# Kernel optimization log

Measured on AMD Instinct MI355X. Metric: run time of the kernel, lower is better.

Reference implementation:

```python
import jax, jax.numpy as jnp
import numpy as np

STRIDES = [4, 8, 16, 32, 64]
SIZES = [32.0, 64.0, 128.0, 256.0, 512.0]
RATIOS = [0.5, 1.0, 2.0]
IMG = 1024.0
PRE_NMS = 1000
POST_NMS = 1000
NMS_THR = 0.7
MIN_SIZE = 0.0
SCALE_CLAMP = float(np.log(1000.0 / 16.0))
NEG = -1e4  # finite sentinel instead of -inf (keeps grads clean)


def conv(x, w, b, pad):
    y = jax.lax.conv_general_dilated(x, w, (1, 1), pad,
                                     dimension_numbers=('NCHW', 'OIHW', 'NCHW'))
    return y + b[None, :, None, None]


def gen_anchors(H, W, stride, size):
    # detectron2 cell anchors: w = size/sqrt(r), h = w*r, centered at shift
    rs = jnp.asarray(RATIOS, jnp.float32)
    ws = size / jnp.sqrt(rs)
    hs = ws * rs
    base = jnp.stack([-ws / 2, -hs / 2, ws / 2, hs / 2], -1)  # [A,4]
    sx = jnp.arange(W, dtype=jnp.float32) * stride
    sy = jnp.arange(H, dtype=jnp.float32) * stride
    shy, shx = jnp.meshgrid(sy, sx, indexing='ij')
    shifts = jnp.stack([shx, shy, shx, shy], -1)  # [H,W,4]
    return (shifts[:, :, None, :] + base[None, None]).reshape(-1, 4)  # [H*W*A,4]


def apply_deltas(d, boxes):
    # Box2BoxTransform.apply_deltas with weights (1,1,1,1)
    w = boxes[..., 2] - boxes[..., 0]
    h = boxes[..., 3] - boxes[..., 1]
    cx = boxes[..., 0] + 0.5 * w
    cy = boxes[..., 1] + 0.5 * h
    dx, dy = d[..., 0], d[..., 1]
    dw = jnp.minimum(d[..., 2], SCALE_CLAMP)
    dh = jnp.minimum(d[..., 3], SCALE_CLAMP)
    pcx = dx * w + cx
    pcy = dy * h + cy
    pw = jnp.exp(dw) * w
    ph = jnp.exp(dh) * h
    return jnp.stack([pcx - 0.5 * pw, pcy - 0.5 * ph,
                      pcx + 0.5 * pw, pcy + 0.5 * ph], -1)


def pairwise_iou(b):
    area = (b[:, 2] - b[:, 0]) * (b[:, 3] - b[:, 1])
    lt = jnp.maximum(b[:, None, :2], b[None, :, :2])
    rb = jnp.minimum(b[:, None, 2:], b[None, :, 2:])
    wh = jnp.clip(rb - lt, 0.0)
    inter = wh[..., 0] * wh[..., 1]
    return inter / (area[:, None] + area[None, :] - inter + 1e-9)


def nms_single(boxes, off_boxes, scores, valid):
    # greedy NMS over score-sorted candidates; off_boxes carry per-level offsets
    order = jnp.argsort(-scores)
    b = boxes[order]
    ob = off_boxes[order]
    s = scores[order]
    v = valid[order]
    M = b.shape[0]
    iou = pairwise_iou(ob)
    sup = (iou > NMS_THR) & jnp.tril(jnp.ones((M, M), bool), -1)

    def step(keep, xs):
        row, vi, i = xs
        ki = vi & jnp.logical_not(jnp.any(keep & row))
        return keep.at[i].set(ki), None

    keep, _ = jax.lax.scan(step, jnp.zeros((M,), bool), (sup, v, jnp.arange(M)))
    ks = jnp.where(keep, s, NEG)
    topv, topi = jax.lax.top_k(ks, POST_NMS)
    return b[topi], topv


def rpn_forward(feats, w_conv, b_conv, w_obj, b_obj, w_delta, b_delta):
    scores, boxes, lvls = [], [], []
    for lvl, (f, st, sz) in enumerate(zip(feats, STRIDES, SIZES)):
        t = jax.nn.relu(conv(f, w_conv, b_conv, 'SAME'))
        logit = conv(t, w_obj, b_obj, 'VALID')   # [N,A,H,W]
        delta = conv(t, w_delta, b_delta, 'VALID')  # [N,4A,H,W]
        N, A, H, W = logit.shape
        logit = logit.transpose(0, 2, 3, 1).reshape(N, H * W * A)
        delta = delta.reshape(N, A, 4, H, W).transpose(0, 3, 4, 1, 2).reshape(N, H * W * A, 4)
        anch = gen_anchors(H, W, st, sz)
        k = min(PRE_NMS, H * W * A)
        ts, ti = jax.lax.top_k(logit, k)  # per-level pre-NMS topk
        td = jnp.take_along_axis(delta, ti[..., None], axis=1)
        ta = anch[ti]
        scores.append(ts)
        boxes.append(apply_deltas(td, ta))
        lvls.append(jnp.full((k,), float(lvl), jnp.float32))
    s = jnp.concatenate(scores, 1)                 # [N, M]
    b = jnp.concatenate(boxes, 1)                  # [N, M, 4]
    l = jnp.concatenate(lvls)                      # [M]
    b = jnp.clip(b, 0.0, IMG)                      # clip to image
    bw = b[..., 2] - b[..., 0]
    bh = b[..., 3] - b[..., 1]
    valid = (bw > MIN_SIZE) & (bh > MIN_SIZE)      # min-size filter as mask
    ob = b + (l * (IMG * 4.0))[None, :, None]      # batched_nms level offsets
    nb, ns = jax.vmap(nms_single, in_axes=(0, 0, 0, 0))(b, ob, s, valid)
    return jnp.concatenate([nb, ns[..., None]], -1)  # [N, POST_NMS, 5]


def setup_inputs() -> dict:
    key = jax.random.key(0)
    ks = jax.random.split(key, 8)
    inp = {
        'feat0': jax.random.normal(ks[0], (2, 256, 256, 256), jnp.float32),
        'feat1': jax.random.normal(ks[1], (2, 256, 128, 128), jnp.float32),
        'feat2': jax.random.normal(ks[2], (2, 256, 64, 64), jnp.float32),
        'feat3': jax.random.normal(ks[3], (2, 256, 32, 32), jnp.float32),
        'feat4': jax.random.normal(ks[4], (2, 256, 16, 16), jnp.float32),
        'w_conv': jax.random.normal(ks[5], (256, 256, 3, 3), jnp.float32) * 0.02,
        'b_conv': jnp.zeros((256,), jnp.float32),
        'w_obj': jax.random.normal(ks[6], (3, 256, 1, 1), jnp.float32) * 0.05,
        'b_obj': jnp.zeros((3,), jnp.float32),
        'w_delta': jax.random.normal(ks[7], (12, 256, 1, 1), jnp.float32) * 0.05,
        'b_delta': jnp.zeros((12,), jnp.float32),
    }
    return inp


def reference(feat0, feat1, feat2, feat3, feat4, w_conv, b_conv, w_obj, b_obj, w_delta, b_delta):
    return rpn_forward([feat0, feat1, feat2, feat3, feat4],
                       w_conv, b_conv, w_obj, b_obj, w_delta, b_delta)
```

## Files before the change

### kernel.cpp

```cpp
#include <hip/hip_runtime.h>
#include <cstdint>
#include <cstddef>

static constexpr int NIMG = 2;
static constexpr int CCH  = 256;
static constexpr int LTOT = 261888;
static constexpr int MCAT = 4768;
static constexpr int MW   = 75;
static constexpr double SCALE_CLAMP_D = 4.135166556742356;

__device__ __forceinline__ unsigned keyd(float f) {
  unsigned u = __float_as_uint(f);
  return (u >> 31) ? ~u : (u | 0x80000000u);
}
__device__ __forceinline__ float invkey(unsigned d) {
  unsigned u = (d & 0x80000000u) ? (d & 0x7FFFFFFFu) : ~d;
  return __uint_as_float(u);
}

__global__ void k_wT(const float* __restrict__ w, float* __restrict__ wT) {
  int i = blockIdx.x * 256 + threadIdx.x;
  if (i >= 2304 * 256) return;
  int co = i & 255;
  int ct = i >> 8;
  wT[ct * 256 + co] = w[co * 2304 + ct];
}

__device__ __forceinline__ void conv_body(
    const float* __restrict__ x, const float* __restrict__ wT,
    const float* __restrict__ bias, float* __restrict__ t,
    int H, int W, int n, int cog, int h0, int w0) {
  __shared__ float xs[8][6][68];
  __shared__ float wsm[8][9][64];
  const int cout0 = cog * 64;
  const int tx = threadIdx.x;
  const int cg8  = tx >> 5;
  const int rw   = (tx >> 3) & 3;
  const int colg = tx & 7;
  const int col0 = colg * 8;

  float acc[8][8];
#pragma unroll
  for (int a = 0; a < 8; ++a)
#pragma unroll
    for (int b = 0; b < 8; ++b) acc[a][b] = 0.f;

  for (int ck = 0; ck < 32; ++ck) {
    for (int i = tx; i < 8 * 6 * 66; i += 256) {
      int ci = i / 396;
      int r  = (i - ci * 396) / 66;
      int c  = i - ci * 396 - r * 66;
      int gh = h0 - 1 + r, gw = w0 - 1 + c;
      float v = 0.f;
      if ((unsigned)gh < (unsigned)H && (unsigned)gw < (unsigned)W)
        v = x[((size_t)(n * CCH + ck * 8 + ci) * H + gh) * W + gw];
      xs[ci][r][c] = v;
    }
    for (int i = tx; i < 8 * 9 * 64; i += 256) {
      int ci = i / 576;
      int rem = i - ci * 576;
      int tap = rem >> 6;
      int co  = rem & 63;
      wsm[ci][tap][co] = wT[((size_t)(ck * 8 + ci) * 9 + tap) * 256 + cout0 + co];
    }
    __syncthreads();

#pragma unroll
    for (int ci = 0; ci < 8; ++ci) {
#pragma unroll
      for (int kh = 0; kh < 3; ++kh) {
        const float* p = &xs[ci][rw + kh][col0];
        float4 a0 = *reinterpret_cast<const float4*>(p);
        float4 a1 = *reinterpret_cast<const float4*>(p + 4);
        float2 a2 = *reinterpret_cast<const float2*>(p + 8);
        float xr[10] = {a0.x, a0.y, a0.z, a0.w, a1.x, a1.y, a1.z, a1.w, a2.x, a2.y};
#pragma unroll
        for (int kw = 0; kw < 3; ++kw) {
          const float* wp = &wsm[ci][kh * 3 + kw][cg8 * 8];
          float4 wa = *reinterpret_cast<const float4*>(wp);
          float4 wb = *reinterpret_cast<const float4*>(wp + 4);
          float wv[8] = {wa.x, wa.y, wa.z, wa.w, wb.x, wb.y, wb.z, wb.w};
#pragma unroll
          for (int co = 0; co < 8; ++co)
#pragma unroll
            for (int cl = 0; cl < 8; ++cl)
              acc[co][cl] = fmaf(xr[cl + kw], wv[co], acc[co][cl]);
        }
      }
    }
    __syncthreads();
  }

  const int h = h0 + rw;
#pragma unroll
  for (int co = 0; co < 8; ++co) {
    int c = cout0 + cg8 * 8 + co;
    float bv = bias[c];
#pragma unroll
    for (int cl = 0; cl < 8; ++cl) {
      int ww = w0 + col0 + cl;
      if (ww < W) {
        float v = acc[co][cl] + bv;
        t[((size_t)(n * CCH + c) * H + h) * W + ww] = v > 0.f ? v : 0.f;
      }
    }
  }
}

__global__ __launch_bounds__(256, 2)
void k_conv0(const float* __restrict__ x, const float* __restrict__ wT,
             const float* __restrict__ bias, float* __restrict__ t) {
  int n = blockIdx.z >> 2, cog = blockIdx.z & 3;
  conv_body(x, wT, bias, t, 256, 256, n, cog, blockIdx.y * 4, blockIdx.x * 64);
}

__global__ __launch_bounds__(256, 2)
void k_conv4(const float* __restrict__ f1, const float* __restrict__ f2,
             const float* __restrict__ f3, const float* __restrict__ f4,
             const float* __restrict__ wT, const float* __restrict__ bias,
             float* __restrict__ t) {
  int b = blockIdx.x;
  const float* x; float* tb; int H, gx, gy, l;
  if (b < 512)      { x = f1; tb = t;            H = 128; gx = 2; gy = 32; l = b; }
  else if (b < 640) { x = f2; tb = t +  8388608; H =  64; gx = 1; gy = 16; l = b - 512; }
  else if (b < 704) { x = f3; tb = t + 10485760; H =  32; gx = 1; gy =  8; l = b - 640; }
  else              { x = f4; tb = t + 11010048; H =  16; gx = 1; gy =  4; l = b - 704; }
  int bx = l % gx;
  int by = (l / gx) % gy;
  int bz = l / (gx * gy);
  int n = bz >> 2, cog = bz & 3;
  conv_body(x, wT, bias, tb, H, H, n, cog, by * 4, bx * 64);
}

__device__ __forceinline__ void heads_body(
    const float* __restrict__ t,
    const float* __restrict__ wobj, const float* __restrict__ bobj,
    const float* __restrict__ wdel, const float* __restrict__ bdel,
    float* __restrict__ logits, float4* __restrict__ deltas,
    int HW, int loff, int n, int p0) {
  __shared__ float wl[15][256];
  __shared__ float bl[15];
  for (int i = threadIdx.x; i < 15 * 256; i += 256) {
    int o = i >> 8, c = i & 255;
    wl[o][c] = (o < 3) ? wobj[o * 256 + c] : wdel[(o - 3) * 256 + c];
  }
  if (threadIdx.x < 15)
    bl[threadIdx.x] = (threadIdx.x < 3) ? bobj[threadIdx.x] : bdel[threadIdx.x - 3];
  __syncthreads();
  if (p0 >= HW) return;

  float4 acc[15];
#pragma unroll
  for (int o = 0; o < 15; ++o) acc[o] = make_float4(0.f, 0.f, 0.f, 0.f);
  const float* tp = t + (size_t)n * CCH * HW + p0;
  for (int c = 0; c < 256; ++c) {
    float4 v = *reinterpret_cast<const float4*>(tp + (size_t)c * HW);
#pragma unroll
    for (int o = 0; o < 15; ++o) {
      float wv = wl[o][c];
      acc[o].x = fmaf(v.x, wv, acc[o].x);
      acc[o].y = fmaf(v.y, wv, acc[o].y);
      acc[o].z = fmaf(v.z, wv, acc[o].z);
      acc[o].w = fmaf(v.w, wv, acc[o].w);
    }
  }
#pragma unroll
  for (int o = 0; o < 15; ++o) {
    float bv = bl[o];
    acc[o].x += bv; acc[o].y += bv; acc[o].z += bv; acc[o].w += bv;
  }

  const float* af = reinterpret_cast<const float*>(acc);
  size_t base = (size_t)n * LTOT + loff + (size_t)p0 * 3;
#pragma unroll
  for (int i2 = 0; i2 < 4; ++i2) {
#pragma unroll
    for (int a = 0; a < 3; ++a) {
      logits[base + i2 * 3 + a] = af[a * 4 + i2];
      deltas[base + i2 * 3 + a] =
          make_float4(af[(3 + a * 4 + 0) * 4 + i2], af[(3 + a * 4 + 1) * 4 + i2],
                      af[(3 + a * 4 + 2) * 4 + i2], af[(3 + a * 4 + 3) * 4 + i2]);
    }
  }
}

__global__ __launch_bounds__(256)
void k_heads0(const float* __restrict__ t,
              const float* __restrict__ wobj, const float* __restrict__ bobj,
              const float* __restrict__ wdel, const float* __restrict__ bdel,
              float* __restrict__ logits, float4* __restrict__ deltas) {
  heads_body(t, wobj, bobj, wdel, bdel, logits, deltas,
             65536, 0, blockIdx.y, (blockIdx.x * 256 + threadIdx.x) * 4);
}

__global__ __launch_bounds__(256)
void k_heads4(const float* __restrict__ t,
              const float* __restrict__ wobj, const float* __restrict__ bobj,
              const float* __restrict__ wdel, const float* __restrict__ bdel,
              float* __restrict__ logits, float4* __restrict__ deltas) {
  int b = blockIdx.x;
  const float* tb; int HW, loff, start;
  if (b < 16)      { tb = t;            HW = 16384; loff = 196608; start = 0;  }
  else if (b < 20) { tb = t +  8388608; HW =  4096; loff = 245760; start = 16; }
  else if (b < 21) { tb = t + 10485760; HW =  1024; loff = 258048; start = 20; }
  else             { tb = t + 11010048; HW =   256; loff = 261120; start = 21; }
  heads_body(tb, wobj, bobj, wdel, bdel, logits, deltas,
             HW, loff, blockIdx.y, ((b - start) * 256 + threadIdx.x) * 4);
}

__global__ __launch_bounds__(1024)
void k_topk(const float* __restrict__ logits, const float4* __restrict__ deltas,
            float* __restrict__ scat, float4* __restrict__ bout,
            double* __restrict__ obout, unsigned* __restrict__ valid) {
  constexpr int   Hs[5]    = {256, 128, 64, 32, 16};
  constexpr int   strd[5]  = {4, 8, 16, 32, 64};
  constexpr float szs[5]   = {32.f, 64.f, 128.f, 256.f, 512.f};
  constexpr int   loffs[5] = {0, 196608, 245760, 258048, 261120};
  constexpr int   Ms[5]    = {196608, 49152, 12288, 3072, 768};
  constexpr int   ksz[5]   = {1000, 1000, 1000, 1000, 768};
  constexpr int   coffs[5] = {0, 1000, 2000, 3000, 4000};

  __shared__ unsigned hist[2048];
  __shared__ unsigned long long cand[1024];
  __shared__ unsigned tie[1024];
  __shared__ unsigned sB1, sC1, sB2, sC2, sDK, sTN;
  __shared__ unsigned cntG, cntT;

  const int task = blockIdx.x;
  const int n = task / 5, lvl = task % 5;
  const int M = Ms[lvl], K = ksz[lvl], loff = loffs[lvl];
  const float* lg = logits + (size_t)n * LTOT + loff;
  const int tid = threadIdx.x;

  for (int i = tid; i < 2048; i += 1024) hist[i] = 0;
  if (tid == 0) { cntG = 0; cntT = 0; }
  __syncthreads();
  for (int i = tid; i < M; i += 1024) atomicAdd(&hist[keyd(lg[i]) >> 21], 1u);
  __syncthreads();
  if (tid == 0) {
    unsigned acc = 0;
    for (int b = 2047; b >= 0; --b) {
      unsigned na = acc + hist[b];
      if (na >= (unsigned)K) { sB1 = (unsigned)b; sC1 = acc; break; }
      acc = na;
    }
  }
  __syncthreads();
  const unsigned B1 = sB1;
  const unsigned rem1 = (unsigned)K - sC1;

  for (int i = tid; i < 2048; i += 1024) hist[i] = 0;
  __syncthreads();
  for (int i = tid; i < M; i += 1024) {
    unsigned d = keyd(lg[i]);
    if ((d >> 21) == B1) atomicAdd(&hist[(d >> 10) & 0x7FFu], 1u);
  }
  __syncthreads();
  if (tid == 0) {
    unsigned acc = 0;
    for (int b = 2047; b >= 0; --b) {
      unsigned na = acc + hist[b];
      if (na >= rem1) { sB2 = (unsigned)b; sC2 = acc; break; }
      acc = na;
    }
  }
  __syncthreads();
  const unsigned B2 = sB2;
  const unsigned rem2 = rem1 - sC2;
  const unsigned pfx = (B1 << 11) | B2;

  for (int i = tid; i < 1024; i += 1024) hist[i] = 0;
  __syncthreads();
  for (int i = tid; i < M; i += 1024) {
    unsigned d = keyd(lg[i]);
    if ((d >> 10) == pfx) atomicAdd(&hist[d & 0x3FFu], 1u);
  }
  __syncthreads();
  if (tid == 0) {
    unsigned acc = 0;
    for (int b = 1023; b >= 0; --b) {
      unsigned na = acc + hist[b];
      if (na >= rem2) { sDK = (pfx << 10) | (unsigned)b; sTN = rem2 - acc; break; }
      acc = na;
    }
  }
  __syncthreads();
  const unsigned dk = sDK;
  const unsigned tneed = sTN;
  const unsigned cg = (unsigned)K - tneed;

  for (int i = tid; i < M; i += 1024) {
    unsigned d = keyd(lg[i]);
    if (d > dk) {
      unsigned p = atomicAdd(&cntG, 1u);
      cand[p] = ((unsigned long long)(~d) << 32) | (unsigned)i;
    } else if (d == dk) {
      unsigned q = atomicAdd(&cntT, 1u);
      if (q < 1024u) tie[q] = (unsigned)i;
    }
  }
  __syncthreads();
  if (tid == 0) {
    int ct = (int)(cntT < 1024u ? cntT : 1024u);
    for (int a = 1; a < ct; ++a) {
      unsigned v = tie[a]; int b = a - 1;
      while (b >= 0 && tie[b] > v) { tie[b + 1] = tie[b]; --b; }
      tie[b + 1] = v;
    }
    for (unsigned q = 0; q < tneed; ++q)
      cand[cg + q] = ((unsigned long long)(~dk) << 32) | tie[q];
  }
  __syncthreads();
  if (tid >= K) cand[tid] = ~0ULL;
  __syncthreads();

  for (unsigned k2 = 2; k2 <= 1024; k2 <<= 1)
    for (unsigned j = k2 >> 1; j > 0; j >>= 1) {
      __syncthreads();
      unsigned i = (unsigned)tid, l = i ^ j;
      if (l > i) {
        unsigned long long a = cand[i], b = cand[l];
        bool up = ((i & k2) == 0);
        if (up ? (a > b) : (a < b)) { cand[i] = b; cand[l] = a; }
      }
    }
  __syncthreads();

  if (tid < K) {
    unsigned long long kk = cand[tid];
    unsigned idx = (unsigned)kk;
    unsigned d = ~(unsigned)(kk >> 32);
    float s = invkey(d);
    int catpos = n * MCAT + coffs[lvl] + tid;
    scat[catpos] = s;

    int a = idx % 3;
    int pix = idx / 3;
    int W = Hs[lvl];
    int hh = pix / W;
    int ww = pix - hh * W;
    float4 d4 = deltas[(size_t)n * LTOT + loff + idx];

    double r  = (a == 0) ? 0.5 : (a == 1 ? 1.0 : 2.0);
    double sz = (double)szs[lvl];
    double cw = sz / sqrt(r);
    double ch = cw * r;
    double cx = (double)(ww * strd[lvl]);
    double cy = (double)(hh * strd[lvl]);
    double dx = (double)d4.x, dy = (double)d4.y;
    double dw = (double)d4.z; if (dw > SCALE_CLAMP_D) dw = SCALE_CLAMP_D;
    double dh = (double)d4.w; if (dh > SCALE_CLAMP_D) dh = SCALE_CLAMP_D;
    double pcx = dx * cw + cx, pcy = dy * ch + cy;
    double pw = exp(dw) * cw,  ph = exp(dh) * ch;
    double x0 = pcx - 0.5 * pw, y0 = pcy - 0.5 * ph;
    double x1 = pcx + 0.5 * pw, y1 = pcy + 0.5 * ph;
    x0 = x0 < 0.0 ? 0.0 : (x0 > 1024.0 ? 1024.0 : x0);
    y0 = y0 < 0.0 ? 0.0 : (y0 > 1024.0 ? 1024.0 : y0);
    x1 = x1 < 0.0 ? 0.0 : (x1 > 1024.0 ? 1024.0 : x1);
    y1 = y1 < 0.0 ? 0.0 : (y1 > 1024.0 ? 1024.0 : y1);
    bool vld = ((x1 - x0) > 0.0) && ((y1 - y0) > 0.0);

    bout[catpos] = make_float4((float)x0, (float)y0, (float)x1, (float)y1);
    double off = (double)lvl * 4096.0;
    double* op = obout + (size_t)catpos * 4;
    op[0] = x0 + off; op[1] = y0 + off; op[2] = x1 + off; op[3] = y1 + off;
    valid[catpos] = vld ? 1u : 0u;
  }
}

__global__ __launch_bounds__(1024)
void k_sort(const float* __restrict__ scat, const float4* __restrict__ b,
            const double* __restrict__ ob, const unsigned* __restrict__ valid,
            float* __restrict__ s_s, float4* __restrict__ b_s,
            double* __restrict__ ob_s, unsigned* __restrict__ valid_s) {
  __shared__ unsigned long long sk[8192];
  const int n = blockIdx.x;
  const int tid = threadIdx.x;
  for (int i = tid; i < 8192; i += 1024)
    sk[i] = (i < MCAT)
      ? ((unsigned long long)(~keyd(scat[n * MCAT + i])) << 32) | (unsigned)i
      : ~0ULL;
  __syncthreads();
  for (unsigned k2 = 2; k2 <= 8192; k2 <<= 1)
    for (unsigned j = k2 >> 1; j > 0; j >>= 1) {
      for (int m = 0; m < 8; ++m) {
        unsigned i = (unsigned)tid + (unsigned)m * 1024u;
        unsigned l = i ^ j;
        if (l > i) {
          unsigned long long a = sk[i], bb = sk[l];
          bool up = ((i & k2) == 0);
          if (up ? (a > bb) : (a < bb)) { sk[i] = bb; sk[l] = a; }
        }
      }
      __syncthreads();
    }
  for (int r = tid; r < MCAT; r += 1024) {
    unsigned long long kk = sk[r];
    unsigned pos = (unsigned)kk;
    unsigned d = ~(unsigned)(kk >> 32);
    s_s[n * MCAT + r] = invkey(d);
    b_s[n * MCAT + r] = b[n * MCAT + pos];
    const double* src = ob + ((size_t)n * MCAT + pos) * 4;
    double* dst = ob_s + ((size_t)n * MCAT + r) * 4;
    dst[0] = src[0]; dst[1] = src[1]; dst[2] = src[2]; dst[3] = src[3];
    valid_s[n * MCAT + r] = valid[n * MCAT + pos];
  }
}

__global__ __launch_bounds__(256)
void k_mask(const double* __restrict__ ob_s, unsigned long long* __restrict__ mask) {
  const int n = blockIdx.y;
  const int i = blockIdx.x;
  const double* bi = ob_s + ((size_t)n * MCAT + i) * 4;
  const double ix0 = bi[0], iy0 = bi[1], ix1 = bi[2], iy1 = bi[3];
  const double ai = (ix1 - ix0) * (iy1 - iy0);
  const int tid = threadIdx.x;
  for (int j0 = 0; j0 < MCAT; j0 += 256) {
    int j = j0 + tid;
    bool sup = false;
    if (j < MCAT && j > i) {
      const double* bj = ob_s + ((size_t)n * MCAT + j) * 4;
      double jx0 = bj[0], jy0 = bj[1], jx1 = bj[2], jy1 = bj[3];
      double aj = (jx1 - jx0) * (jy1 - jy0);
      double lx = ix0 > jx0 ? ix0 : jx0;
      double ly = iy0 > jy0 ? iy0 : jy0;
      double rx = ix1 < jx1 ? ix1 : jx1;
      double ry = iy1 < jy1 ? iy1 : jy1;
      double wx = rx - lx; wx = wx > 0.0 ? wx : 0.0;
      double wy = ry - ly; wy = wy > 0.0 ? wy : 0.0;
      double inter = wx * wy;
      double iou = inter / (ai + aj - inter + 1e-9);
      sup = iou > 0.7;
    }
    unsigned long long bal = __ballot(sup);
    if ((tid & 63) == 0) {
      int word = (j0 + tid) >> 6;
      if (word < MW) mask[((size_t)n * MCAT + i) * MW + word] = bal;
    }
  }
}

__global__ __launch_bounds__(256)
void k_nms(const unsigned long long* __restrict__ mask,
           const unsigned* __restrict__ valid_s,
           const float* __restrict__ s_s, const float4* __restrict__ b_s,
           float* __restrict__ out) {
  __shared__ unsigned long long rem[MW];
  __shared__ unsigned long long supcc[64];
  __shared__ unsigned long long keepw[MW];
  __shared__ int kl[64];
  __shared__ int snk;
  __shared__ unsigned kpfx[MW], nkpfx[MW];
  __shared__ unsigned sKept;
  const int n = blockIdx.x;
  const int tid = threadIdx.x;
  const unsigned long long* msk = mask + (size_t)n * MCAT * MW;

  for (int w = tid; w < MW; w += 256) {
    unsigned long long r = 0ULL;
    for (int b = 0; b < 64; ++b) {
      int i = w * 64 + b;
      bool rm = (i >= MCAT) || (valid_s[n * MCAT + i] == 0u);
      if (rm) r |= (1ULL << b);
    }
    rem[w] = r;
    keepw[w] = 0ULL;
  }
  __syncthreads();

  for (int c = 0; c < MW; ++c) {
    if (tid < 64) {
      int i = c * 64 + tid;
      supcc[tid] = (i < MCAT) ? msk[(size_t)i * MW + c] : 0ULL;
    }
    __syncthreads();
    if (tid == 0) {
      unsigned long long r = rem[c], km = 0ULL;
      int nk = 0;
      for (int b = 0; b < 64; ++b) {
        if (!((r >> b) & 1ULL)) { km |= (1ULL << b); kl[nk++] = b; r |= supcc[b]; }
      }
      rem[c] = r; keepw[c] = km; snk = nk;
    }
    __syncthreads();
    const int nk = snk;
    const int nw = MW - 1 - c;
    const int total = nk * nw;
    for (int idx = tid; idx < total; idx += 256) {
      int b = kl[idx / nw];
      int w = c + 1 + (idx % nw);
      unsigned long long v = msk[(size_t)(c * 64 + b) * MW + w];
      if (v) atomicOr(&rem[w], v);
    }
    __syncthreads();
  }

  if (tid == 0) {
    unsigned ka = 0, na = 0;
    for (int w = 0; w < MW; ++w) {
      kpfx[w] = ka; nkpfx[w] = na;
      unsigned long long range = (w < MW - 1) ? ~0ULL : ((1ULL << 32) - 1ULL);
      ka += (unsigned)__popcll(keepw[w]);
      na += (unsigned)__popcll((~keepw[w]) & range);
    }
    sKept = ka;
  }
  __syncthreads();
  const unsigned keptTotal = sKept;

  for (int i = tid; i < MCAT; i += 256) {
    int w = i >> 6, b = i & 63;
    unsigned long long below = (1ULL << b) - 1ULL;
    bool kept = (keepw[w] >> b) & 1ULL;
    unsigned row;
    if (kept)
      row = kpfx[w] + (unsigned)__popcll(keepw[w] & below);
    else
      row = keptTotal + nkpfx[w] + (unsigned)__popcll((~keepw[w]) & below);
    if (row < 1000u) {
      float4 bb = b_s[n * MCAT + i];
      float sc = kept ? s_s[n * MCAT + i] : -1e4f;
      float* o = out + ((size_t)n * 1000 + row) * 5;
      o[0] = bb.x; o[1] = bb.y; o[2] = bb.z; o[3] = bb.w; o[4] = sc;
    }
  }
}

extern "C" void kernel_launch(void* const* d_in, const int* in_sizes, int n_in,
                              void* d_out, int out_size, void* d_ws, size_t ws_size,
                              hipStream_t stream) {
  (void)in_sizes; (void)n_in; (void)out_size;
  const float* feats[5] = {(const float*)d_in[0], (const float*)d_in[1],
                           (const float*)d_in[2], (const float*)d_in[3],
                           (const float*)d_in[4]};
  const float* w_conv = (const float*)d_in[5];
  const float* b_conv = (const float*)d_in[6];
  const float* w_obj  = (const float*)d_in[7];
  const float* b_obj  = (const float*)d_in[8];
  const float* w_del  = (const float*)d_in[9];
  const float* b_del  = (const float*)d_in[10];
  float* out = (float*)d_out;

  char* p = (char*)d_ws;
  auto alloc = [&](size_t bytes) -> void* {
    void* r = (void*)p;
    p += (bytes + 255) & ~(size_t)255;
    return r;
  };
  float*  t       = (float*)  alloc((size_t)2 * 256 * 256 * 256 * 4);
  float*  wT      = (float*)  alloc((size_t)2304 * 256 * 4);
  float*  logits  = (float*)  alloc((size_t)NIMG * LTOT * 4);
  float4* deltas  = (float4*) alloc((size_t)NIMG * LTOT * 16);
  float*  scat    = (float*)  alloc((size_t)NIMG * MCAT * 4);
  float4* bout    = (float4*) alloc((size_t)NIMG * MCAT * 16);
  double* obout   = (double*) alloc((size_t)NIMG * MCAT * 32);
  unsigned* valid = (unsigned*)alloc((size_t)NIMG * MCAT * 4);
  float*  s_s     = (float*)  alloc((size_t)NIMG * MCAT * 4);
  float4* b_s     = (float4*) alloc((size_t)NIMG * MCAT * 16);
  double* ob_s    = (double*) alloc((size_t)NIMG * MCAT * 32);
  unsigned* val_s = (unsigned*)alloc((size_t)NIMG * MCAT * 4);
  unsigned long long* mask =
      (unsigned long long*)alloc((size_t)NIMG * MCAT * MW * 8);
  if ((size_t)(p - (char*)d_ws) > ws_size) return;

  k_wT<<<2304, 256, 0, stream>>>(w_conv, wT);

  k_conv4<<<736, 256, 0, stream>>>(feats[1], feats[2], feats[3], feats[4],
                                   wT, b_conv, t);
  k_heads4<<<dim3(22, 2), 256, 0, stream>>>(t, w_obj, b_obj, w_del, b_del,
                                            logits, deltas);
  k_conv0<<<dim3(4, 64, 8), 256, 0, stream>>>(feats[0], wT, b_conv, t);
  k_heads0<<<dim3(64, 2), 256, 0, stream>>>(t, w_obj, b_obj, w_del, b_del,
                                            logits, deltas);

  k_topk<<<10, 1024, 0, stream>>>(logits, deltas, scat, bout, obout, valid);
  k_sort<<<2, 1024, 0, stream>>>(scat, bout, obout, valid, s_s, b_s, ob_s, val_s);
  k_mask<<<dim3(MCAT, 2), 256, 0, stream>>>(ob_s, mask);
  k_nms<<<2, 256, 0, stream>>>(mask, val_s, s_s, b_s, out);
}
```

Before: 4.947 ms.

## Retile conv3x3 thread mapping to 4 channels x 16 pixels per thread

Changes each thread's register tile in the 3x3 convolution from 8 output channels x 8 pixels to 4 channels x 16 pixels. Each thread now reads 18 input values and 4 weights from shared memory per tap. The input shared tile is padded to 76 columns, and the load loops are restructured per input channel. Launch bounds rise from 2 to 3 blocks per SM, trading registers for occupancy, which risks spills and more weight reads per FMA.

```diff
diff --git a/kernel.cpp b/kernel.cpp
--- a/kernel.cpp
+++ b/kernel.cpp
@@ -9,6 +9,7 @@
 static constexpr int MW   = 75;
 static constexpr double SCALE_CLAMP_D = 4.135166556742356;
 
+
 __device__ __forceinline__ unsigned keyd(float f) {
   unsigned u = __float_as_uint(f);
   return (u >> 31) ? ~u : (u | 0x80000000u);
@@ -30,38 +31,40 @@
     const float* __restrict__ x, const float* __restrict__ wT,
     const float* __restrict__ bias, float* __restrict__ t,
     int H, int W, int n, int cog, int h0, int w0) {
-  __shared__ float xs[8][6][68];
-  __shared__ float wsm[8][9][64];
+  __shared__ __align__(16) float xs[8][6][76];
+  __shared__ __align__(16) float wsm[8][9][64];
   const int cout0 = cog * 64;
   const int tx = threadIdx.x;
-  const int cg8  = tx >> 5;
-  const int rw   = (tx >> 3) & 3;
-  const int colg = tx & 7;
-  const int col0 = colg * 8;
-
-  float acc[8][8];
-#pragma unroll
-  for (int a = 0; a < 8; ++a)
-#pragma unroll
-    for (int b = 0; b < 8; ++b) acc[a][b] = 0.f;
+  const int cog4 = tx >> 4;
+  const int pxg  = tx & 15;
+  const int r2   = pxg >> 2;
+  const int col0 = (pxg & 3) * 16;
+
+  float acc[4][16];
+#pragma unroll
+  for (int a = 0; a < 4; ++a)
+#pragma unroll
+    for (int b = 0; b < 16; ++b) acc[a][b] = 0.f;
 
   for (int ck = 0; ck < 32; ++ck) {
-    for (int i = tx; i < 8 * 6 * 66; i += 256) {
-      int ci = i / 396;
-      int r  = (i - ci * 396) / 66;
-      int c  = i - ci * 396 - r * 66;
-      int gh = h0 - 1 + r, gw = w0 - 1 + c;
-      float v = 0.f;
-      if ((unsigned)gh < (unsigned)H && (unsigned)gw < (unsigned)W)
-        v = x[((size_t)(n * CCH + ck * 8 + ci) * H + gh) * W + gw];
-      xs[ci][r][c] = v;
-    }
-    for (int i = tx; i < 8 * 9 * 64; i += 256) {
-      int ci = i / 576;
-      int rem = i - ci * 576;
-      int tap = rem >> 6;
-      int co  = rem & 63;
-      wsm[ci][tap][co] = wT[((size_t)(ck * 8 + ci) * 9 + tap) * 256 + cout0 + co];
+#pragma unroll
+    for (int ci = 0; ci < 8; ++ci) {
+      const float* xc = x + (size_t)(n * CCH + ck * 8 + ci) * H * W;
+      for (int e = tx; e < 396; e += 256) {
+        int r = e / 66, c = e - r * 66;
+        int gh = h0 - 1 + r, gw = w0 - 1 + c;
+        float v = 0.f;
+        if ((unsigned)gh < (unsigned)H && (unsigned)gw < (unsigned)W)
+          v = xc[gh * W + gw];
+        xs[ci][r][c] = v;
+      }
+    }
+#pragma unroll
+    for (int ci = 0; ci < 8; ++ci) {
+      for (int e = tx; e < 576; e += 256) {
+        int tap = e >> 6, co = e & 63;
+        wsm[ci][tap][co] = wT[((size_t)(ck * 8 + ci) * 9 + tap) * 256 + cout0 + co];
+      }
     }
     __syncthreads();
 
@@ -69,52 +72,54 @@
     for (int ci = 0; ci < 8; ++ci) {
 #pragma unroll
       for (int kh = 0; kh < 3; ++kh) {
-        const float* p = &xs[ci][rw + kh][col0];
+        const float* p = &xs[ci][r2 + kh][col0];
         float4 a0 = *reinterpret_cast<const float4*>(p);
         float4 a1 = *reinterpret_cast<const float4*>(p + 4);
-        float2 a2 = *reinterpret_cast<const float2*>(p + 8);
-        float xr[10] = {a0.x, a0.y, a0.z, a0.w, a1.x, a1.y, a1.z, a1.w, a2.x, a2.y};
+        float4 a2 = *reinterpret_cast<const float4*>(p + 8);
+        float4 a3 = *reinterpret_cast<const float4*>(p + 12);
+        float2 a4 = *reinterpret_cast<const float2*>(p + 16);
+        float xr[18] = {a0.x, a0.y, a0.z, a0.w, a1.x, a1.y, a1.z, a1.w,
+                        a2.x, a2.y, a2.z, a2.w, a3.x, a3.y, a3.z, a3.w,
+                        a4.x, a4.y};
 #pragma unroll
         for (int kw = 0; kw < 3; ++kw) {
-          const float* wp = &wsm[ci][kh * 3 + kw][cg8 * 8];
-          float4 wa = *reinterpret_cast<const float4*>(wp);
-          float4 wb = *reinterpret_cast<const float4*>(wp + 4);
-          float wv[8] = {wa.x, wa.y, wa.z, wa.w, wb.x, wb.y, wb.z, wb.w};
-#pragma unroll
-          for (int co = 0; co < 8; ++co)
-#pragma unroll
-            for (int cl = 0; cl < 8; ++cl)
-              acc[co][cl] = fmaf(xr[cl + kw], wv[co], acc[co][cl]);
+          float4 wq = *reinterpret_cast<const float4*>(&wsm[ci][kh * 3 + kw][cog4 * 4]);
+          float wv[4] = {wq.x, wq.y, wq.z, wq.w};
+#pragma unroll
+          for (int co = 0; co < 4; ++co)
+#pragma unroll
+            for (int j = 0; j < 16; ++j)
+              acc[co][j] = fmaf(xr[j + kw], wv[co], acc[co][j]);
         }
       }
     }
     __syncthreads();
   }
 
-  const int h = h0 + rw;
-#pragma unroll
-  for (int co = 0; co < 8; ++co) {
-    int c = cout0 + cg8 * 8 + co;
+  const int h = h0 + r2;
+#pragma unroll
+  for (int co = 0; co < 4; ++co) {
+    int c = cout0 + cog4 * 4 + co;
     float bv = bias[c];
 #pragma unroll
-    for (int cl = 0; cl < 8; ++cl) {
-      int ww = w0 + col0 + cl;
+    for (int j = 0; j < 16; ++j) {
+      int ww = w0 + col0 + j;
       if (ww < W) {
-        float v = acc[co][cl] + bv;
+        float v = acc[co][j] + bv;
         t[((size_t)(n * CCH + c) * H + h) * W + ww] = v > 0.f ? v : 0.f;
       }
     }
   }
 }
 
-__global__ __launch_bounds__(256, 2)
+__global__ __launch_bounds__(256, 3)
 void k_conv0(const float* __restrict__ x, const float* __restrict__ wT,
              const float* __restrict__ bias, float* __restrict__ t) {
   int n = blockIdx.z >> 2, cog = blockIdx.z & 3;
   conv_body(x, wT, bias, t, 256, 256, n, cog, blockIdx.y * 4, blockIdx.x * 64);
 }
 
-__global__ __launch_bounds__(256, 2)
+__global__ __launch_bounds__(256, 3)
 void k_conv4(const float* __restrict__ f1, const float* __restrict__ f2,
              const float* __restrict__ f3, const float* __restrict__ f4,
              const float* __restrict__ wT, const float* __restrict__ bias,
```

Result: faster. 4.543 ms (-8.2%).
